# Kernel optimization log

Hardware: AMD Instinct MI355X
Metric: run time of the kernel (lower is better)

## Reference

```python
import jax, jax.numpy as jnp
import numpy as np
import math

DIM = 4096
N_HEADS = 32
N_KV_HEADS = 8
HEAD_DIM = DIM // N_HEADS          # 128
N_REP = N_HEADS // N_KV_HEADS      # 4
BATCH = 2
SEQ = 2048
ROPE_THETA = 10000.0


def rope_cos_sin(seq_len, head_dim, theta=ROPE_THETA):
    # matches precompute_freqs_cis: freqs over even indices, outer with positions
    inv_freq = 1.0 / (theta ** (jnp.arange(0, head_dim, 2, dtype=jnp.float32) / head_dim))
    t = jnp.arange(seq_len, dtype=jnp.float32)
    ang = jnp.outer(t, inv_freq)          # [S, head_dim//2]
    return jnp.cos(ang), jnp.sin(ang)


def apply_rope(x, cos, sin):
    # x: [B, S, H, D]; consecutive pairs (x0, x1) form complex numbers (view_as_complex)
    x0 = x[..., 0::2]
    x1 = x[..., 1::2]
    c = cos[None, :, None, :]
    s = sin[None, :, None, :]
    r0 = x0 * c - x1 * s
    r1 = x0 * s + x1 * c
    return jnp.stack([r0, r1], axis=-1).reshape(x.shape)


def setup_inputs() -> dict:
    key = jax.random.key(0)
    ks = jax.random.split(key, 5)
    scale = 1.0 / math.sqrt(DIM)
    return {
        "x": jax.random.normal(ks[0], (BATCH, SEQ, DIM), dtype=jnp.float32),
        "wq": jax.random.normal(ks[1], (DIM, N_HEADS * HEAD_DIM), dtype=jnp.float32) * scale,
        "wk": jax.random.normal(ks[2], (DIM, N_KV_HEADS * HEAD_DIM), dtype=jnp.float32) * scale,
        "wv": jax.random.normal(ks[3], (DIM, N_KV_HEADS * HEAD_DIM), dtype=jnp.float32) * scale,
        "wo": jax.random.normal(ks[4], (N_HEADS * HEAD_DIM, DIM), dtype=jnp.float32) * scale,
        "start_pos": 0,
    }


def reference(x, wq, wk, wv, wo, start_pos):
    B, S, _ = x.shape
    # projections
    q = (x @ wq).reshape(B, S, N_HEADS, HEAD_DIM)
    k = (x @ wk).reshape(B, S, N_KV_HEADS, HEAD_DIM)
    v = (x @ wv).reshape(B, S, N_KV_HEADS, HEAD_DIM)
    # RoPE on q, k (training path: full-sequence freqs)
    cos, sin = rope_cos_sin(S, HEAD_DIM)
    q = apply_rope(q, cos, sin)
    k = apply_rope(k, cos, sin)
    # GQA: repeat_kv expands kv heads by n_rep
    k = jnp.repeat(k, N_REP, axis=2)  # [B, S, H, D]
    v = jnp.repeat(v, N_REP, axis=2)
    # [B, H, S, D]
    q = q.transpose(0, 2, 1, 3)
    k = k.transpose(0, 2, 1, 3)
    v = v.transpose(0, 2, 1, 3)
    scores = jnp.einsum("bhqd,bhkd->bhqk", q, k) / math.sqrt(HEAD_DIM)
    # causal mask: -inf above diagonal
    mask = jnp.triu(jnp.full((S, S), float("-inf"), dtype=scores.dtype), k=1)
    scores = scores + mask[None, None]
    attn = jax.nn.softmax(scores.astype(jnp.float32), axis=-1).astype(q.dtype)
    out = jnp.einsum("bhqk,bhkd->bhqd", attn, v)
    out = out.transpose(0, 2, 1, 3).reshape(B, S, N_HEADS * HEAD_DIM)
    return out @ wo
```

## Files before the change

### kernel.cpp

```cpp
#include <hip/hip_runtime.h>

#define DIM 4096
#define HD 128
#define NH 32
#define NKV 8
#define SEQ 2048
#define BATCH 2
#define MTOT (BATCH*SEQ)
#define GK DIM

typedef __bf16 bf16;
typedef __bf16 bf16x4 __attribute__((ext_vector_type(4)));
typedef __bf16 bf16x8 __attribute__((ext_vector_type(8)));
typedef float f32x4 __attribute__((ext_vector_type(4)));

__device__ __forceinline__ void gload_lds16(const void* g, void* l) {
    __builtin_amdgcn_global_load_lds(
        (const __attribute__((address_space(1))) void*)g,
        (__attribute__((address_space(3))) void*)l, 16, 0, 0);
}

__global__ __launch_bounds__(256) void conv_bf16(const float* __restrict__ in,
                                                 bf16* __restrict__ out, int n8) {
    int i = blockIdx.x * 256 + threadIdx.x;
    if (i >= n8) return;
    const float4* p = (const float4*)(in + (size_t)i * 8);
    float4 a = p[0], b = p[1];
    bf16x8 v;
    v[0]=(bf16)a.x; v[1]=(bf16)a.y; v[2]=(bf16)a.z; v[3]=(bf16)a.w;
    v[4]=(bf16)b.x; v[5]=(bf16)b.y; v[6]=(bf16)b.z; v[7]=(bf16)b.w;
    *(bf16x8*)(out + (size_t)i * 8) = v;
}

__global__ __launch_bounds__(256) void tconv(const float* __restrict__ in,
                                             bf16* __restrict__ out, int N, int K) {
    __shared__ float t[32][33];
    int bx = blockIdx.x, by = blockIdx.y;
    int tx = threadIdx.x, ty = threadIdx.y;
    int col = bx * 32 + tx;
#pragma unroll
    for (int r = 0; r < 4; ++r) {
        int row = by * 32 + ty + r * 8;
        t[ty + r * 8][tx] = in[(size_t)row * N + col];
    }
    __syncthreads();
#pragma unroll
    for (int r = 0; r < 4; ++r) {
        int n = bx * 32 + ty + r * 8;
        int k = by * 32 + tx;
        out[(size_t)n * K + k] = (bf16)t[tx][ty + r * 8];
    }
}

__global__ __launch_bounds__(256) void rope_k(bf16* __restrict__ buf, int shift, int n8) {
    int i = blockIdx.x * 256 + threadIdx.x;
    if (i >= n8) return;
    size_t base = (size_t)i * 8;
    int col = (int)(base & ((1u << shift) - 1));
    int pos = (int)((base >> shift) & (SEQ - 1));
    int d0 = col & (HD - 1);
    bf16x8 v = *(const bf16x8*)(buf + base);
    float f[8];
#pragma unroll
    for (int j = 0; j < 8; ++j) f[j] = (float)v[j];
    const float nl2t = -13.287712379549449f / 64.f;
#pragma unroll
    for (int j = 0; j < 4; ++j) {
        float inv = exp2f(nl2t * (float)((d0 >> 1) + j));
        float ang = (float)pos * inv;
        float sn, cs;
        sincosf(ang, &sn, &cs);
        float x0 = f[2 * j], x1 = f[2 * j + 1];
        f[2 * j]     = x0 * cs - x1 * sn;
        f[2 * j + 1] = x0 * sn + x1 * cs;
    }
    bf16x8 ov;
#pragma unroll
    for (int j = 0; j < 8; ++j) ov[j] = (bf16)f[j];
    *(bf16x8*)(buf + base) = ov;
}

template <bool F32OUT>
__global__ __launch_bounds__(256) void gemm_bt(const bf16* __restrict__ A,
                                               const bf16* __restrict__ Bt,
                                               void* __restrict__ out0, int N) {
    __shared__ alignas(16) bf16 sA[2][128 * 32];
    __shared__ alignas(16) bf16 sB[2][128 * 32];
    const int tid = threadIdx.x;
    const int lane = tid & 63, wid = tid >> 6;
    const int wm = wid >> 1, wn = wid & 1;
    const int m0 = blockIdx.y * 128, n0 = blockIdx.x * 128;

    auto stage = [&](int buf, int kt) {
#pragma unroll
        for (int it = 0; it < 2; ++it) {
            int slot = it * 256 + tid;
            int row = slot >> 2, s = slot & 3;
            gload_lds16(A + (size_t)(m0 + row) * GK + kt * 32 + s * 8, &sA[buf][slot * 8]);
            gload_lds16(Bt + (size_t)(n0 + row) * GK + kt * 32 + s * 8, &sB[buf][slot * 8]);
        }
    };

    f32x4 acc[4][4] = {};
    stage(0, 0);
    __syncthreads();
    int cur = 0;
    for (int kt = 0; kt < GK / 32; ++kt) {
        if (kt + 1 < GK / 32) stage(cur ^ 1, kt + 1);
        bf16x8 aF[4], bF[4];
#pragma unroll
        for (int i = 0; i < 4; ++i) {
            aF[i] = *(const bf16x8*)&sA[cur][(wm * 64 + i * 16 + (lane & 15)) * 32 + (lane >> 4) * 8];
            bF[i] = *(const bf16x8*)&sB[cur][(wn * 64 + i * 16 + (lane & 15)) * 32 + (lane >> 4) * 8];
        }
#pragma unroll
        for (int mi = 0; mi < 4; ++mi)
#pragma unroll
            for (int ni = 0; ni < 4; ++ni)
                acc[mi][ni] = __builtin_amdgcn_mfma_f32_16x16x32_bf16(aF[mi], bF[ni], acc[mi][ni], 0, 0, 0);
        __syncthreads();
        cur ^= 1;
    }
#pragma unroll
    for (int mi = 0; mi < 4; ++mi) {
#pragma unroll
        for (int ni = 0; ni < 4; ++ni) {
#pragma unroll
            for (int r = 0; r < 4; ++r) {
                int row = m0 + wm * 64 + mi * 16 + (lane >> 4) * 4 + r;
                int col = n0 + wn * 64 + ni * 16 + (lane & 15);
                float v = acc[mi][ni][r];
                if constexpr (F32OUT) {
                    ((float*)out0)[(size_t)row * N + col] = v;
                } else {
                    ((bf16*)out0)[(size_t)row * N + col] = (bf16)v;
                }
            }
        }
    }
}

template <bool F32OUT>
__global__ __launch_bounds__(512, 2) void gemm8(const bf16* __restrict__ A,
                                                const bf16* __restrict__ Bt,
                                                void* __restrict__ outp, int N) {
    __shared__ alignas(16) char sA[2][2][16384];
    __shared__ alignas(16) char sB[2][2][16384];
    const int tid = threadIdx.x, lane = tid & 63;
    const int wid = tid >> 6;
    const int wm = wid >> 2, wn = wid & 3;
    const int m0 = blockIdx.y * 256, n0 = blockIdx.x * 256;
    const int lrow = lane & 15, hc = lane >> 4;
    const int rowbase = ((lrow >> 1) * 128) +
                        (((((lrow & 1) << 2) | hc) ^ (lrow >> 1)) << 4);
    const int NT = GK / 64;

    auto stageK = [&](int t, int kh) {
        if (t >= NT) return;
        const int b = t & 1;
#pragma unroll
        for (int it = 0; it < 2; ++it) {
            int sl = it * 512 + tid;
            int PRr = sl >> 3, ps = sl & 7;
            int lsl = ps ^ (PRr & 7);
            int r = PRr * 2 + (lsl >> 2);
            int cc = lsl & 3;
            size_t koff = (size_t)t * 64 + kh * 32 + cc * 8;
            gload_lds16(A + (size_t)(m0 + r) * GK + koff, &sA[b][kh][sl * 16]);
            gload_lds16(Bt + (size_t)(n0 + r) * GK + koff, &sB[b][kh][sl * 16]);
        }
    };

    f32x4 acc[8][4] = {};

    stageK(0, 0); stageK(0, 1); stageK(1, 0); stageK(1, 1);
    asm volatile("s_waitcnt vmcnt(12)" ::: "memory");
    __builtin_amdgcn_s_barrier();

    for (int t = 0; t < NT; ++t) {
        const int b = t & 1;
        const char* Ab = &sA[b][0][0];
        const char* Bb = &sB[b][0][0];
        bf16x8 af[8], bfr[2];

#pragma unroll
        for (int mi = 0; mi < 8; ++mi)
            af[mi] = *(const bf16x8*)(Ab + wm * 8192 + mi * 1024 + rowbase);
        bfr[0] = *(const bf16x8*)(Bb + wn * 4096 + 0 * 1024 + rowbase);
        bfr[1] = *(const bf16x8*)(Bb + wn * 4096 + 1 * 1024 + rowbase);
        if (t > 0) stageK(t + 1, 1);
        __builtin_amdgcn_s_barrier();
        asm volatile("s_waitcnt lgkmcnt(0)" ::: "memory");
        __builtin_amdgcn_sched_barrier(0);
        __builtin_amdgcn_s_setprio(1);
#pragma unroll
        for (int mi = 0; mi < 8; ++mi) {
            acc[mi][0] = __builtin_amdgcn_mfma_f32_16x16x32_bf16(af[mi], bfr[0], acc[mi][0], 0, 0, 0);
            acc[mi][1] = __builtin_amdgcn_mfma_f32_16x16x32_bf16(af[mi], bfr[1], acc[mi][1], 0, 0, 0);
        }
        __builtin_amdgcn_s_setprio(0);
        __builtin_amdgcn_s_barrier();

        bfr[0] = *(const bf16x8*)(Bb + wn * 4096 + 2 * 1024 + rowbase);
        bfr[1] = *(const bf16x8*)(Bb + wn * 4096 + 3 * 1024 + rowbase);
        __builtin_amdgcn_s_barrier();
        asm volatile("s_waitcnt lgkmcnt(0)" ::: "memory");
        __builtin_amdgcn_sched_barrier(0);
        __builtin_amdgcn_s_setprio(1);
#pragma unroll
        for (int mi = 0; mi < 8; ++mi) {
            acc[mi][2] = __builtin_amdgcn_mfma_f32_16x16x32_bf16(af[mi], bfr[0], acc[mi][2], 0, 0, 0);
            acc[mi][3] = __builtin_amdgcn_mfma_f32_16x16x32_bf16(af[mi], bfr[1], acc[mi][3], 0, 0, 0);
        }
        __builtin_amdgcn_s_setprio(0);
        asm volatile("s_waitcnt vmcnt(8)" ::: "memory");
        __builtin_amdgcn_s_barrier();

#pragma unroll
        for (int mi = 0; mi < 8; ++mi)
            af[mi] = *(const bf16x8*)(Ab + 16384 + wm * 8192 + mi * 1024 + rowbase);
        bfr[0] = *(const bf16x8*)(Bb + 16384 + wn * 4096 + 0 * 1024 + rowbase);
        bfr[1] = *(const bf16x8*)(Bb + 16384 + wn * 4096 + 1 * 1024 + rowbase);
        stageK(t + 2, 0);
        __builtin_amdgcn_s_barrier();
        asm volatile("s_waitcnt lgkmcnt(0)" ::: "memory");
        __builtin_amdgcn_sched_barrier(0);
        __builtin_amdgcn_s_setprio(1);
#pragma unroll
        for (int mi = 0; mi < 8; ++mi) {
            acc[mi][0] = __builtin_amdgcn_mfma_f32_16x16x32_bf16(af[mi], bfr[0], acc[mi][0], 0, 0, 0);
            acc[mi][1] = __builtin_amdgcn_mfma_f32_16x16x32_bf16(af[mi], bfr[1], acc[mi][1], 0, 0, 0);
        }
        __builtin_amdgcn_s_setprio(0);
        __builtin_amdgcn_s_barrier();

        bfr[0] = *(const bf16x8*)(Bb + 16384 + wn * 4096 + 2 * 1024 + rowbase);
        bfr[1] = *(const bf16x8*)(Bb + 16384 + wn * 4096 + 3 * 1024 + rowbase);
        __builtin_amdgcn_s_barrier();
        asm volatile("s_waitcnt lgkmcnt(0)" ::: "memory");
        __builtin_amdgcn_sched_barrier(0);
        __builtin_amdgcn_s_setprio(1);
#pragma unroll
        for (int mi = 0; mi < 8; ++mi) {
            acc[mi][2] = __builtin_amdgcn_mfma_f32_16x16x32_bf16(af[mi], bfr[0], acc[mi][2], 0, 0, 0);
            acc[mi][3] = __builtin_amdgcn_mfma_f32_16x16x32_bf16(af[mi], bfr[1], acc[mi][3], 0, 0, 0);
        }
        __builtin_amdgcn_s_setprio(0);
        asm volatile("s_waitcnt vmcnt(8)" ::: "memory");
        __builtin_amdgcn_s_barrier();
    }

#pragma unroll
    for (int mi = 0; mi < 8; ++mi)
#pragma unroll
        for (int ni = 0; ni < 4; ++ni)
#pragma unroll
            for (int r = 0; r < 4; ++r) {
                int row = m0 + wm * 128 + mi * 16 + hc * 4 + r;
                int col = n0 + wn * 64 + ni * 16 + lrow;
                if constexpr (F32OUT)
                    ((float*)outp)[(size_t)row * N + col] = acc[mi][ni][r];
                else
                    ((bf16*)outp)[(size_t)row * N + col] = (bf16)acc[mi][ni][r];
            }
}

__global__ __launch_bounds__(512, 4) void attn_fwd(const bf16* __restrict__ q,
                                                   const bf16* __restrict__ k,
                                                   const bf16* __restrict__ vt,
                                                   bf16* __restrict__ o) {
    __shared__ alignas(16) bf16 sK[2][64 * 128];
    __shared__ alignas(16) bf16 sV[2][128 * 64];
    __shared__ alignas(16) bf16 sP[8][16 * 64];
    const int tid = threadIdx.x, lane = tid & 63, wid = tid >> 6;
    const int bi = blockIdx.x;
    const int pr = bi & 7;
    const int h = (bi >> 3) & 31;
    const int b = bi >> 8;
    const int kvh = h >> 2;
    const float scale = 0.08838834764831845f;

    const bf16* kb0 = k + (size_t)b * SEQ * (NKV * HD) + kvh * HD;
    const bf16* vb0 = vt + (size_t)(kvh * HD) * MTOT + (size_t)b * SEQ;

    auto stage = [&](int bf, int tt) {
#pragma unroll
        for (int it = 0; it < 2; ++it) {
            int slot = it * 512 + tid;
            int row = slot >> 4, s = slot & 15;
            gload_lds16(kb0 + (size_t)(tt * 64 + row) * (NKV * HD) + ((s ^ (row & 7)) * 8),
                        &sK[bf][slot * 8]);
        }
#pragma unroll
        for (int it = 0; it < 2; ++it) {
            int slot = it * 512 + tid;
            int row = slot >> 3, s = slot & 7;
            gload_lds16(vb0 + (size_t)row * MTOT + tt * 64 + ((s ^ (row & 7)) * 8),
                        &sV[bf][slot * 8]);
        }
    };

    auto pass = [&](int qt) {
        const int qb0 = qt * 128;
        const int nt = 2 * qt + 2;
        const bf16* qp = q + ((size_t)(b * SEQ + qb0 + wid * 16 + (lane & 15))) * DIM
                           + h * HD + (lane >> 4) * 8;
        bf16x8 aQ[4];
#pragma unroll
        for (int ks = 0; ks < 4; ++ks) aQ[ks] = *(const bf16x8*)(qp + ks * 32);

        f32x4 accO[8] = {};
        float m_r = -1e30f, l_r = 0.f;
        const int qglob = qb0 + wid * 16 + (lane & 15);
        char* pb = (char*)&sP[wid][0];
        const int q7s = (lane & 7) << 4;
        const int hi = lane >> 4;

        stage(0, 0);
        __syncthreads();
        int cur = 0;
        for (int tt = 0; tt < nt; ++tt) {
            if (tt + 1 < nt) stage(cur ^ 1, tt + 1);
            if (tt * 64 <= qb0 + wid * 16 + 15) {
                f32x4 accS[4] = {};
#pragma unroll
                for (int nt2 = 0; nt2 < 4; ++nt2) {
                    int kr = nt2 * 16 + (lane & 15);
#pragma unroll
                    for (int ks = 0; ks < 4; ++ks) {
                        int slog = ks * 4 + hi;
                        bf16x8 bK = *(const bf16x8*)&sK[cur][kr * 128 + ((slog ^ (kr & 7)) * 8)];
                        accS[nt2] = __builtin_amdgcn_mfma_f32_16x16x32_bf16(bK, aQ[ks], accS[nt2], 0, 0, 0);
                    }
                }

                const bool diag = (tt * 64 + 63 > qb0 + wid * 16);
                const int kvb = tt * 64 + hi * 4;
                float mx = -1e30f;
#pragma unroll
                for (int nt2 = 0; nt2 < 4; ++nt2)
#pragma unroll
                    for (int r = 0; r < 4; ++r) {
                        float v = accS[nt2][r] * scale;
                        if (diag && (kvb + nt2 * 16 + r > qglob)) v = -1e30f;
                        accS[nt2][r] = v;
                        mx = fmaxf(mx, v);
                    }
                mx = fmaxf(mx, __shfl_xor(mx, 16, 64));
                mx = fmaxf(mx, __shfl_xor(mx, 32, 64));

                float mn = fmaxf(m_r, mx);
                float al = __expf(m_r - mn);
                m_r = mn;
                float rs = 0.f;
#pragma unroll
                for (int nt2 = 0; nt2 < 4; ++nt2)
#pragma unroll
                    for (int r = 0; r < 4; ++r) {
                        float p = __expf(accS[nt2][r] - mn);
                        accS[nt2][r] = p;
                        rs += p;
                    }
                rs += __shfl_xor(rs, 16, 64);
                rs += __shfl_xor(rs, 32, 64);
                l_r = l_r * al + rs;

                float al4[4];
#pragma unroll
                for (int r = 0; r < 4; ++r) al4[r] = __shfl(al, hi * 4 + r, 64);
#pragma unroll
                for (int d2 = 0; d2 < 8; ++d2)
#pragma unroll
                    for (int r = 0; r < 4; ++r) accO[d2][r] *= al4[r];

#pragma unroll
                for (int nt2 = 0; nt2 < 4; ++nt2) {
                    bf16x4 pv;
                    pv[0] = (bf16)accS[nt2][0]; pv[1] = (bf16)accS[nt2][1];
                    pv[2] = (bf16)accS[nt2][2]; pv[3] = (bf16)accS[nt2][3];
                    *(bf16x4*)(pb + (lane & 15) * 128 + ((nt2 * 32 + hi * 8) ^ q7s)) = pv;
                }

                bf16x8 aP[2];
#pragma unroll
                for (int kk = 0; kk < 2; ++kk)
                    aP[kk] = *(const bf16x8*)(pb + (lane & 15) * 128 + ((kk * 64 + hi * 16) ^ q7s));
#pragma unroll
                for (int d2 = 0; d2 < 8; ++d2) {
#pragma unroll
                    for (int kk = 0; kk < 2; ++kk) {
                        int dv = d2 * 16 + (lane & 15);
                        int phys = (kk * 4 + hi) ^ (dv & 7);
                        bf16x8 bV = *(const bf16x8*)&sV[cur][dv * 64 + phys * 8];
                        accO[d2] = __builtin_amdgcn_mfma_f32_16x16x32_bf16(aP[kk], bV, accO[d2], 0, 0, 0);
                    }
                }
            }
            __syncthreads();
            cur ^= 1;
        }

        float linv[4];
#pragma unroll
        for (int r = 0; r < 4; ++r) linv[r] = 1.f / __shfl(l_r, hi * 4 + r, 64);
        size_t orow = (size_t)(b * SEQ + qb0 + wid * 16 + hi * 4) * DIM
                    + h * HD + (lane & 15);
#pragma unroll
        for (int d2 = 0; d2 < 8; ++d2)
#pragma unroll
            for (int r = 0; r < 4; ++r)
                o[orow + (size_t)r * DIM + d2 * 16] = (bf16)(accO[d2][r] * linv[r]);
    };

    pass(pr);
    pass(15 - pr);
}

extern "C" void kernel_launch(void* const* d_in, const int* in_sizes, int n_in,
                              void* d_out, int out_size, void* d_ws, size_t ws_size,
                              hipStream_t stream) {
    const float* x  = (const float*)d_in[0];
    const float* wq = (const float*)d_in[1];
    const float* wk = (const float*)d_in[2];
    const float* wv = (const float*)d_in[3];
    const float* wo = (const float*)d_in[4];
    float* out = (float*)d_out;

    char* ws = (char*)d_ws;
    size_t off = 0;
    bf16* xb  = (bf16*)(ws + off); off += (size_t)MTOT * DIM * 2;
    bf16* wqt = (bf16*)(ws + off); off += (size_t)DIM * DIM * 2;
    bf16* wkt = (bf16*)(ws + off); off += (size_t)1024 * DIM * 2;
    bf16* wvt = (bf16*)(ws + off); off += (size_t)1024 * DIM * 2;
    bf16* qb  = (bf16*)(ws + off); off += (size_t)MTOT * DIM * 2;
    bf16* kb  = (bf16*)(ws + off); off += (size_t)MTOT * 1024 * 2;
    bf16* vtb = (bf16*)(ws + off); off += (size_t)MTOT * 1024 * 2;
    bf16* ao = xb;

    dim3 tb(32, 8);
    conv_bf16<<<(MTOT * DIM / 8) / 256, 256, 0, stream>>>(x, xb, MTOT * DIM / 8);
    tconv<<<dim3(DIM / 32, DIM / 32), tb, 0, stream>>>(wq, wqt, DIM, DIM);
    tconv<<<dim3(1024 / 32, DIM / 32), tb, 0, stream>>>(wk, wkt, 1024, DIM);
    tconv<<<dim3(1024 / 32, DIM / 32), tb, 0, stream>>>(wv, wvt, 1024, DIM);

    gemm8<false><<<dim3(DIM / 256, MTOT / 256), 512, 0, stream>>>(xb, wqt, qb, DIM);
    gemm_bt<false><<<dim3(1024 / 128, MTOT / 128), 256, 0, stream>>>(xb, wkt, kb, 1024);
    gemm_bt<false><<<dim3(MTOT / 128, 1024 / 128), 256, 0, stream>>>(wvt, xb, vtb, MTOT);

    rope_k<<<(MTOT * DIM / 8) / 256, 256, 0, stream>>>(qb, 12, MTOT * DIM / 8);
    rope_k<<<(MTOT * 1024 / 8) / 256, 256, 0, stream>>>(kb, 10, MTOT * 1024 / 8);

    tconv<<<dim3(DIM / 32, DIM / 32), tb, 0, stream>>>(wo, wqt, DIM, DIM);

    attn_fwd<<<BATCH * NH * 8, 512, 0, stream>>>(qb, kb, vtb, ao);

    gemm8<true><<<dim3(DIM / 256, MTOT / 256), 512, 0, stream>>>(ao, wqt, out, DIM);
}
```

Baseline: 621.6 us.

## Restructure gemm8 main loop into per-half-K stages with single barrier

Rewrites the 256x256 GEMM main loop so each 32-wide K half loads all 4 B and 8 A fragments at once, then issues 32 MFMAs in one block. The previous version split the work into four MFMA phases with several barriers each. Prefetch now runs one tile ahead per half (stageR t+1) instead of two, and each half uses a single vmcnt wait plus one barrier. The smaller gemm kernel also reorders its LDS fragment reads, loading B before A. The change cuts barrier and waitcnt overhead but holds more fragment registers at once and has a shallower prefetch distance, which may expose global-load latency.

```diff
diff --git a/kernel.cpp b/kernel.cpp
--- a/kernel.cpp
+++ b/kernel.cpp
@@ -107,12 +107,13 @@
     int cur = 0;
     for (int kt = 0; kt < GK / 32; ++kt) {
         if (kt + 1 < GK / 32) stage(cur ^ 1, kt + 1);
-        bf16x8 aF[4], bF[4];
-#pragma unroll
-        for (int i = 0; i < 4; ++i) {
+        bf16x8 bF[4], aF[4];
+#pragma unroll
+        for (int i = 0; i < 4; ++i)
+            bF[i] = *(const bf16x8*)&sB[cur][(wn * 64 + i * 16 + (lane & 15)) * 32 + (lane >> 4) * 8];
+#pragma unroll
+        for (int i = 0; i < 4; ++i)
             aF[i] = *(const bf16x8*)&sA[cur][(wm * 64 + i * 16 + (lane & 15)) * 32 + (lane >> 4) * 8];
-            bF[i] = *(const bf16x8*)&sB[cur][(wn * 64 + i * 16 + (lane & 15)) * 32 + (lane >> 4) * 8];
-        }
 #pragma unroll
         for (int mi = 0; mi < 4; ++mi)
 #pragma unroll
@@ -155,9 +156,7 @@
                         (((((lrow & 1) << 2) | hc) ^ (lrow >> 1)) << 4);
     const int NT = GK / 64;
 
-    auto stageK = [&](int t, int kh) {
-        if (t >= NT) return;
-        const int b = t & 1;
+    auto stageR = [&](int t, int kh) {
 #pragma unroll
         for (int it = 0; it < 2; ++it) {
             int sl = it * 512 + tid;
@@ -166,88 +165,45 @@
             int r = PRr * 2 + (lsl >> 2);
             int cc = lsl & 3;
             size_t koff = (size_t)t * 64 + kh * 32 + cc * 8;
-            gload_lds16(A + (size_t)(m0 + r) * GK + koff, &sA[b][kh][sl * 16]);
-            gload_lds16(Bt + (size_t)(n0 + r) * GK + koff, &sB[b][kh][sl * 16]);
+            gload_lds16(A + (size_t)(m0 + r) * GK + koff, &sA[t & 1][kh][sl * 16]);
+            gload_lds16(Bt + (size_t)(n0 + r) * GK + koff, &sB[t & 1][kh][sl * 16]);
         }
     };
 
     f32x4 acc[8][4] = {};
 
-    stageK(0, 0); stageK(0, 1); stageK(1, 0); stageK(1, 1);
-    asm volatile("s_waitcnt vmcnt(12)" ::: "memory");
+    stageR(0, 0); stageR(0, 1);
+    asm volatile("s_waitcnt vmcnt(4)" ::: "memory");
     __builtin_amdgcn_s_barrier();
 
     for (int t = 0; t < NT; ++t) {
-        const int b = t & 1;
-        const char* Ab = &sA[b][0][0];
-        const char* Bb = &sB[b][0][0];
-        bf16x8 af[8], bfr[2];
-
-#pragma unroll
-        for (int mi = 0; mi < 8; ++mi)
-            af[mi] = *(const bf16x8*)(Ab + wm * 8192 + mi * 1024 + rowbase);
-        bfr[0] = *(const bf16x8*)(Bb + wn * 4096 + 0 * 1024 + rowbase);
-        bfr[1] = *(const bf16x8*)(Bb + wn * 4096 + 1 * 1024 + rowbase);
-        if (t > 0) stageK(t + 1, 1);
-        __builtin_amdgcn_s_barrier();
-        asm volatile("s_waitcnt lgkmcnt(0)" ::: "memory");
-        __builtin_amdgcn_sched_barrier(0);
-        __builtin_amdgcn_s_setprio(1);
-#pragma unroll
-        for (int mi = 0; mi < 8; ++mi) {
-            acc[mi][0] = __builtin_amdgcn_mfma_f32_16x16x32_bf16(af[mi], bfr[0], acc[mi][0], 0, 0, 0);
-            acc[mi][1] = __builtin_amdgcn_mfma_f32_16x16x32_bf16(af[mi], bfr[1], acc[mi][1], 0, 0, 0);
-        }
-        __builtin_amdgcn_s_setprio(0);
-        __builtin_amdgcn_s_barrier();
-
-        bfr[0] = *(const bf16x8*)(Bb + wn * 4096 + 2 * 1024 + rowbase);
-        bfr[1] = *(const bf16x8*)(Bb + wn * 4096 + 3 * 1024 + rowbase);
-        __builtin_amdgcn_s_barrier();
-        asm volatile("s_waitcnt lgkmcnt(0)" ::: "memory");
-        __builtin_amdgcn_sched_barrier(0);
-        __builtin_amdgcn_s_setprio(1);
-#pragma unroll
-        for (int mi = 0; mi < 8; ++mi) {
-            acc[mi][2] = __builtin_amdgcn_mfma_f32_16x16x32_bf16(af[mi], bfr[0], acc[mi][2], 0, 0, 0);
-            acc[mi][3] = __builtin_amdgcn_mfma_f32_16x16x32_bf16(af[mi], bfr[1], acc[mi][3], 0, 0, 0);
-        }
-        __builtin_amdgcn_s_setprio(0);
-        asm volatile("s_waitcnt vmcnt(8)" ::: "memory");
-        __builtin_amdgcn_s_barrier();
-
-#pragma unroll
-        for (int mi = 0; mi < 8; ++mi)
-            af[mi] = *(const bf16x8*)(Ab + 16384 + wm * 8192 + mi * 1024 + rowbase);
-        bfr[0] = *(const bf16x8*)(Bb + 16384 + wn * 4096 + 0 * 1024 + rowbase);
-        bfr[1] = *(const bf16x8*)(Bb + 16384 + wn * 4096 + 1 * 1024 + rowbase);
-        stageK(t + 2, 0);
-        __builtin_amdgcn_s_barrier();
-        asm volatile("s_waitcnt lgkmcnt(0)" ::: "memory");
-        __builtin_amdgcn_sched_barrier(0);
-        __builtin_amdgcn_s_setprio(1);
-#pragma unroll
-        for (int mi = 0; mi < 8; ++mi) {
-            acc[mi][0] = __builtin_amdgcn_mfma_f32_16x16x32_bf16(af[mi], bfr[0], acc[mi][0], 0, 0, 0);
-            acc[mi][1] = __builtin_amdgcn_mfma_f32_16x16x32_bf16(af[mi], bfr[1], acc[mi][1], 0, 0, 0);
-        }
-        __builtin_amdgcn_s_setprio(0);
-        __builtin_amdgcn_s_barrier();
-
-        bfr[0] = *(const bf16x8*)(Bb + 16384 + wn * 4096 + 2 * 1024 + rowbase);
-        bfr[1] = *(const bf16x8*)(Bb + 16384 + wn * 4096 + 3 * 1024 + rowbase);
-        __builtin_amdgcn_s_barrier();
-        asm volatile("s_waitcnt lgkmcnt(0)" ::: "memory");
-        __builtin_amdgcn_sched_barrier(0);
-        __builtin_amdgcn_s_setprio(1);
-#pragma unroll
-        for (int mi = 0; mi < 8; ++mi) {
-            acc[mi][2] = __builtin_amdgcn_mfma_f32_16x16x32_bf16(af[mi], bfr[0], acc[mi][2], 0, 0, 0);
-            acc[mi][3] = __builtin_amdgcn_mfma_f32_16x16x32_bf16(af[mi], bfr[1], acc[mi][3], 0, 0, 0);
-        }
-        __builtin_amdgcn_s_setprio(0);
-        asm volatile("s_waitcnt vmcnt(8)" ::: "memory");
-        __builtin_amdgcn_s_barrier();
+#pragma unroll
+        for (int kh = 0; kh < 2; ++kh) {
+            const char* Ab = &sA[t & 1][kh][0];
+            const char* Bb = &sB[t & 1][kh][0];
+            bf16x8 bf[4], af[8];
+#pragma unroll
+            for (int ni = 0; ni < 4; ++ni)
+                bf[ni] = *(const bf16x8*)(Bb + wn * 4096 + ni * 1024 + rowbase);
+#pragma unroll
+            for (int mi = 0; mi < 8; ++mi)
+                af[mi] = *(const bf16x8*)(Ab + wm * 8192 + mi * 1024 + rowbase);
+            if (t + 1 < NT) {
+                stageR(t + 1, kh);
+                asm volatile("s_waitcnt vmcnt(4)" ::: "memory");
+            } else {
+                asm volatile("s_waitcnt vmcnt(0)" ::: "memory");
+            }
+            __builtin_amdgcn_s_barrier();
+            __builtin_amdgcn_sched_barrier(0);
+            __builtin_amdgcn_s_setprio(1);
+#pragma unroll
+            for (int mi = 0; mi < 8; ++mi)
+#pragma unroll
+                for (int ni = 0; ni < 4; ++ni)
+                    acc[mi][ni] = __builtin_amdgcn_mfma_f32_16x16x32_bf16(af[mi], bf[ni], acc[mi][ni], 0, 0, 0);
+            __builtin_amdgcn_s_setprio(0);
+        }
     }
 
 #pragma unroll
```

New measurement: 627.6 us. About the same (+1.0%).
